# Kernel tuning notes

Hardware: AMD Instinct MI355X
Metric: run time of the kernel (lower is better)

## Reference

```python
import jax, jax.numpy as jnp
import numpy as np

BN_EPS = 1e-5

def setup_inputs() -> dict:
    key = jax.random.key(0)
    ks = jax.random.split(key, 6)
    N, D, H = 1024, 256, 128
    scale = 0.05
    return {
        "graph_embeddings": jax.random.normal(ks[0], (N, D), jnp.float32),
        "W1": jax.random.normal(ks[1], (2 * D, H), jnp.float32) * scale,
        "b1": jnp.zeros((H,), jnp.float32),
        "W2": jax.random.normal(ks[2], (H, 1), jnp.float32) * scale,
        "b2": jnp.zeros((1,), jnp.float32),
        "Wg": jax.random.normal(ks[3], (D, H), jnp.float32) * scale,
        "bg": jnp.zeros((H,), jnp.float32),
        "gamma": jnp.ones((H,), jnp.float32),
        "beta": jnp.zeros((H,), jnp.float32),
    }

def reference(graph_embeddings, W1, b1, W2, b2, Wg, bg, gamma, beta):
    N, D = graph_embeddings.shape
    # Pairwise similarity MLP: sim(i,j) = sigmoid(W2 @ relu(W1 @ [x_i; x_j] + b1) + b2)
    # Split W1 over the concat dim so we never materialize [N,N,2D].
    a = graph_embeddings @ W1[:D]          # [N, H] contribution of x_i
    c = graph_embeddings @ W1[D:]          # [N, H] contribution of x_j
    h = jax.nn.relu(a[:, None, :] + c[None, :, :] + b1)   # [N, N, H]
    sim = jax.nn.sigmoid(jnp.einsum('ijh,h->ij', h, W2[:, 0]) + b2[0])  # [N, N]
    # Torch loop uses sim(i,j) with i<j for both directions; keep edge iff sim > 0.5.
    U = jnp.triu(sim, k=1)
    A = jnp.where(U > 0.5, U, 0.0)
    A = A + A.T + jnp.eye(N, dtype=sim.dtype)  # symmetric + GCN self-loops (weight 1)
    # GCN symmetric normalization: D^{-1/2} A D^{-1/2}
    deg = A.sum(axis=1)
    dis = jax.lax.rsqrt(deg)
    A_hat = A * dis[:, None] * dis[None, :]
    out = A_hat @ (graph_embeddings @ Wg) + bg  # [N, H]
    # BatchNorm1d (training mode: batch stats, biased variance)
    mean = out.mean(axis=0)
    var = out.var(axis=0)
    out = gamma * (out - mean) * jax.lax.rsqrt(var + BN_EPS) + beta
    return jax.nn.relu(out)
```

## Files before the change

### kernel.cpp

```cpp
#include <hip/hip_runtime.h>
#include <math.h>

constexpr int NN = 1024;
constexpr int DD = 256;
constexpr int HH = 128;
constexpr float BN_EPS = 1e-5f;

constexpr int OFF_A      = 0;
constexpr int OFF_AP     = OFF_A + NN * NN;
constexpr int OFF_CP     = OFF_AP + NN * HH;
constexpr int OFF_Y      = OFF_CP + NN * HH;
constexpr int OFF_DIS    = OFF_Y + NN * HH;
constexpr int OFF_STATS  = OFF_DIS + NN;
constexpr int OFF_OUTPRE = OFF_STATS + 256;
constexpr int OFF_P4     = OFF_OUTPRE + NN * HH;

__global__ __launch_bounds__(256) void k1_gemm(
    const float* __restrict__ X, const float* __restrict__ W1,
    const float* __restrict__ Wg, const float* __restrict__ b1,
    float* __restrict__ aP, float* __restrict__ cP, float* __restrict__ y) {
  __shared__ float xs[16 * 256];
  __shared__ float ws[64 * 128];
  const int tid = threadIdx.x;
  const int i0 = blockIdx.x * 16;
  const int m = blockIdx.y;
  const float* W = (m == 0) ? W1 : (m == 1 ? W1 + DD * HH : Wg);
  const float* Xbase = X + i0 * DD;
#pragma unroll
  for (int v = 0; v < 4; ++v) {
    const int fi = (v * 256 + tid) * 4;
    *(float4*)(xs + fi) = *(const float4*)(Xbase + fi);
  }
  const int tx = tid & 31, ty = tid >> 5;
  float4 acc0 = make_float4(0.f, 0.f, 0.f, 0.f);
  float4 acc1 = make_float4(0.f, 0.f, 0.f, 0.f);
  for (int c = 0; c < 4; ++c) {
    __syncthreads();
    const float* Wbase = W + c * 64 * HH;
#pragma unroll
    for (int v = 0; v < 8; ++v) {
      const int fi = (v * 256 + tid) * 4;
      *(float4*)(ws + fi) = *(const float4*)(Wbase + fi);
    }
    __syncthreads();
    const float* xr0 = xs + (ty * 2) * 256 + c * 64;
    const float* xr1 = xs + (ty * 2 + 1) * 256 + c * 64;
#pragma unroll 4
    for (int d = 0; d < 64; d += 4) {
      const float4 x0 = *(const float4*)(xr0 + d);
      const float4 x1 = *(const float4*)(xr1 + d);
      const float4 w0 = *(const float4*)(ws + (d + 0) * 128 + tx * 4);
      const float4 w1 = *(const float4*)(ws + (d + 1) * 128 + tx * 4);
      const float4 w2 = *(const float4*)(ws + (d + 2) * 128 + tx * 4);
      const float4 w3 = *(const float4*)(ws + (d + 3) * 128 + tx * 4);
      acc0.x = fmaf(x0.x, w0.x, acc0.x); acc0.y = fmaf(x0.x, w0.y, acc0.y);
      acc0.z = fmaf(x0.x, w0.z, acc0.z); acc0.w = fmaf(x0.x, w0.w, acc0.w);
      acc1.x = fmaf(x1.x, w0.x, acc1.x); acc1.y = fmaf(x1.x, w0.y, acc1.y);
      acc1.z = fmaf(x1.x, w0.z, acc1.z); acc1.w = fmaf(x1.x, w0.w, acc1.w);
      acc0.x = fmaf(x0.y, w1.x, acc0.x); acc0.y = fmaf(x0.y, w1.y, acc0.y);
      acc0.z = fmaf(x0.y, w1.z, acc0.z); acc0.w = fmaf(x0.y, w1.w, acc0.w);
      acc1.x = fmaf(x1.y, w1.x, acc1.x); acc1.y = fmaf(x1.y, w1.y, acc1.y);
      acc1.z = fmaf(x1.y, w1.z, acc1.z); acc1.w = fmaf(x1.y, w1.w, acc1.w);
      acc0.x = fmaf(x0.z, w2.x, acc0.x); acc0.y = fmaf(x0.z, w2.y, acc0.y);
      acc0.z = fmaf(x0.z, w2.z, acc0.z); acc0.w = fmaf(x0.z, w2.w, acc0.w);
      acc1.x = fmaf(x1.z, w2.x, acc1.x); acc1.y = fmaf(x1.z, w2.y, acc1.y);
      acc1.z = fmaf(x1.z, w2.z, acc1.z); acc1.w = fmaf(x1.z, w2.w, acc1.w);
      acc0.x = fmaf(x0.w, w3.x, acc0.x); acc0.y = fmaf(x0.w, w3.y, acc0.y);
      acc0.z = fmaf(x0.w, w3.z, acc0.z); acc0.w = fmaf(x0.w, w3.w, acc0.w);
      acc1.x = fmaf(x1.w, w3.x, acc1.x); acc1.y = fmaf(x1.w, w3.y, acc1.y);
      acc1.z = fmaf(x1.w, w3.z, acc1.z); acc1.w = fmaf(x1.w, w3.w, acc1.w);
    }
  }
  float* dst = (m == 0) ? aP : (m == 1 ? cP : y);
  if (m == 0) {
    const float4 bv = *(const float4*)(b1 + tx * 4);
    acc0.x += bv.x; acc0.y += bv.y; acc0.z += bv.z; acc0.w += bv.w;
    acc1.x += bv.x; acc1.y += bv.y; acc1.z += bv.z; acc1.w += bv.w;
  }
  const int r0 = i0 + ty * 2;
  *(float4*)(dst + r0 * HH + tx * 4) = acc0;
  *(float4*)(dst + (r0 + 1) * HH + tx * 4) = acc1;
}

__global__ __launch_bounds__(256) void k2_pairwise(
    const float* __restrict__ aP, const float* __restrict__ cP,
    const float* __restrict__ W2, const float* __restrict__ b2,
    float* __restrict__ A) {
  const int ti = blockIdx.x, tj = blockIdx.y;
  if (tj < ti) return;
  __shared__ float as[32 * 132];
  __shared__ float cs[32 * 132];
  __shared__ float es[32 * 33];
  const int tid = threadIdx.x;
  const int i0 = ti * 32, j0 = tj * 32;
  for (int idx = tid; idx < 32 * HH; idx += 256) {
    const int row = idx >> 7, col = idx & 127;
    as[row * 132 + col] = aP[(i0 + row) * HH + col];
    cs[row * 132 + col] = cP[(j0 + row) * HH + col];
  }
  __syncthreads();
  const int li0 = (tid >> 4) * 2, lj0 = (tid & 15) * 2;
  float s00 = 0.f, s01 = 0.f, s10 = 0.f, s11 = 0.f;
#pragma unroll 8
  for (int h = 0; h < HH; h += 4) {
    const float4 a0 = *(const float4*)(as + li0 * 132 + h);
    const float4 a1 = *(const float4*)(as + (li0 + 1) * 132 + h);
    const float4 c0 = *(const float4*)(cs + lj0 * 132 + h);
    const float4 c1 = *(const float4*)(cs + (lj0 + 1) * 132 + h);
    const float4 w = *(const float4*)(W2 + h);
    s00 += fmaxf(a0.x + c0.x, 0.f) * w.x + fmaxf(a0.y + c0.y, 0.f) * w.y +
           fmaxf(a0.z + c0.z, 0.f) * w.z + fmaxf(a0.w + c0.w, 0.f) * w.w;
    s01 += fmaxf(a0.x + c1.x, 0.f) * w.x + fmaxf(a0.y + c1.y, 0.f) * w.y +
           fmaxf(a0.z + c1.z, 0.f) * w.z + fmaxf(a0.w + c1.w, 0.f) * w.w;
    s10 += fmaxf(a1.x + c0.x, 0.f) * w.x + fmaxf(a1.y + c0.y, 0.f) * w.y +
           fmaxf(a1.z + c0.z, 0.f) * w.z + fmaxf(a1.w + c0.w, 0.f) * w.w;
    s11 += fmaxf(a1.x + c1.x, 0.f) * w.x + fmaxf(a1.y + c1.y, 0.f) * w.y +
           fmaxf(a1.z + c1.z, 0.f) * w.z + fmaxf(a1.w + c1.w, 0.f) * w.w;
  }
  const float b2v = b2[0];
  auto edge = [b2v](float s) {
    s += b2v;
    return s > 0.f ? 1.f / (1.f + __expf(-s)) : 0.f;
  };
  es[(li0 + 0) * 33 + lj0 + 0] = edge(s00);
  es[(li0 + 0) * 33 + lj0 + 1] = edge(s01);
  es[(li0 + 1) * 33 + lj0 + 0] = edge(s10);
  es[(li0 + 1) * 33 + lj0 + 1] = edge(s11);
  __syncthreads();
  if (ti == tj) {
#pragma unroll
    for (int r = 0; r < 2; ++r)
#pragma unroll
      for (int t = 0; t < 2; ++t) {
        const int li = li0 + r, lj = lj0 + t;
        const float v =
            (li == lj) ? 1.f : (li < lj ? es[li * 33 + lj] : es[lj * 33 + li]);
        A[(i0 + li) * NN + j0 + lj] = v;
      }
  } else {
#pragma unroll
    for (int r = 0; r < 2; ++r)
#pragma unroll
      for (int t = 0; t < 2; ++t) {
        const int li = li0 + r, lj = lj0 + t;
        A[(i0 + li) * NN + j0 + lj] = es[li * 33 + lj];
        A[(j0 + li) * NN + i0 + lj] = es[lj * 33 + li];
      }
  }
}

__global__ __launch_bounds__(256) void k3_deg(
    const float* __restrict__ A, float* __restrict__ dis,
    float* __restrict__ stats) {
  const int i = blockIdx.x;
  const int tid = threadIdx.x;
  if (i == 0) stats[tid] = 0.f;
  const float4 v = *(const float4*)(A + i * NN + tid * 4);
  float s = v.x + v.y + v.z + v.w;
#pragma unroll
  for (int off = 32; off > 0; off >>= 1) s += __shfl_down(s, off, 64);
  __shared__ float sm[4];
  if ((tid & 63) == 0) sm[tid >> 6] = s;
  __syncthreads();
  if (tid == 0) dis[i] = rsqrtf(sm[0] + sm[1] + sm[2] + sm[3]);
}

__global__ __launch_bounds__(256) void k4_spmm_partial(
    const float* __restrict__ A, const float* __restrict__ Y,
    const float* __restrict__ dis, float* __restrict__ P4) {
  __shared__ float At[128 * 36];
  __shared__ float ys[32 * 128];
  const int tid = threadIdx.x;
  const int i0 = blockIdx.x * 32;
  const int jc = blockIdx.y * 128;
  for (int idx = tid; idx < 32 * 128; idx += 256) {
    const int col = idx & 127, row = idx >> 7;
    At[col * 36 + row] = A[(i0 + row) * NN + jc + col];
  }
  const int tx = tid & 31, ty = tid >> 5;
  float4 acc[4];
#pragma unroll
  for (int r = 0; r < 4; ++r) acc[r] = make_float4(0.f, 0.f, 0.f, 0.f);
  for (int s = 0; s < 4; ++s) {
    __syncthreads();
#pragma unroll
    for (int v = 0; v < 4; ++v) {
      const int fi = (v * 256 + tid) * 4;
      const int r = fi >> 7, col = fi & 127;
      float4 t = *(const float4*)(Y + (jc + s * 32 + r) * HH + col);
      const float dv = dis[jc + s * 32 + r];
      t.x *= dv; t.y *= dv; t.z *= dv; t.w *= dv;
      *(float4*)(ys + fi) = t;
    }
    __syncthreads();
#pragma unroll 8
    for (int jj = 0; jj < 32; ++jj) {
      const float4 av = *(const float4*)(At + (s * 32 + jj) * 36 + ty * 4);
      const float4 yv = *(const float4*)(ys + jj * 128 + tx * 4);
      acc[0].x = fmaf(av.x, yv.x, acc[0].x); acc[0].y = fmaf(av.x, yv.y, acc[0].y);
      acc[0].z = fmaf(av.x, yv.z, acc[0].z); acc[0].w = fmaf(av.x, yv.w, acc[0].w);
      acc[1].x = fmaf(av.y, yv.x, acc[1].x); acc[1].y = fmaf(av.y, yv.y, acc[1].y);
      acc[1].z = fmaf(av.y, yv.z, acc[1].z); acc[1].w = fmaf(av.y, yv.w, acc[1].w);
      acc[2].x = fmaf(av.z, yv.x, acc[2].x); acc[2].y = fmaf(av.z, yv.y, acc[2].y);
      acc[2].z = fmaf(av.z, yv.z, acc[2].z); acc[2].w = fmaf(av.z, yv.w, acc[2].w);
      acc[3].x = fmaf(av.w, yv.x, acc[3].x); acc[3].y = fmaf(av.w, yv.y, acc[3].y);
      acc[3].z = fmaf(av.w, yv.z, acc[3].z); acc[3].w = fmaf(av.w, yv.w, acc[3].w);
    }
  }
  const int bc = blockIdx.y;
#pragma unroll
  for (int r = 0; r < 4; ++r) {
    const int i = i0 + ty * 4 + r;
    *(float4*)(P4 + bc * (NN * HH) + i * HH + tx * 4) = acc[r];
  }
}

__global__ __launch_bounds__(256) void k5a_reduce_stats(
    const float* __restrict__ P4, const float* __restrict__ dis,
    const float* __restrict__ bg, float* __restrict__ out_pre,
    float* __restrict__ stats) {
  const int tid = threadIdx.x;
  const int h = tid & 127, rg = tid >> 7;
  const int i0 = blockIdx.x * 8;
  float ls = 0.f, lq = 0.f;
  const float bgv = bg[h];
#pragma unroll
  for (int r = rg; r < 8; r += 2) {
    const int i = i0 + r;
    float v = 0.f;
#pragma unroll
    for (int s = 0; s < 8; ++s) v += P4[s * (NN * HH) + i * HH + h];
    v = v * dis[i] + bgv;
    out_pre[i * HH + h] = v;
    ls += v;
    lq += v * v;
  }
  __shared__ float sm1[2][128], sm2[2][128];
  sm1[rg][h] = ls;
  sm2[rg][h] = lq;
  __syncthreads();
  if (rg == 0) {
    atomicAdd(&stats[h], sm1[0][h] + sm1[1][h]);
    atomicAdd(&stats[128 + h], sm2[0][h] + sm2[1][h]);
  }
}

__global__ __launch_bounds__(256) void k5b_bn(
    const float* __restrict__ out_pre, const float* __restrict__ stats,
    const float* __restrict__ gamma, const float* __restrict__ beta,
    float* __restrict__ out) {
  const int idx = blockIdx.x * 256 + threadIdx.x;
  const int h = idx & 127;
  const float mean = stats[h] * (1.f / NN);
  const float var = stats[128 + h] * (1.f / NN) - mean * mean;
  float v = (out_pre[idx] - mean) * rsqrtf(var + BN_EPS);
  v = gamma[h] * v + beta[h];
  out[idx] = fmaxf(v, 0.f);
}

extern "C" void kernel_launch(void* const* d_in, const int* in_sizes, int n_in,
                              void* d_out, int out_size, void* d_ws,
                              size_t ws_size, hipStream_t stream) {
  const float* X = (const float*)d_in[0];
  const float* W1 = (const float*)d_in[1];
  const float* b1 = (const float*)d_in[2];
  const float* W2 = (const float*)d_in[3];
  const float* b2 = (const float*)d_in[4];
  const float* Wg = (const float*)d_in[5];
  const float* bg = (const float*)d_in[6];
  const float* gamma = (const float*)d_in[7];
  const float* beta = (const float*)d_in[8];
  float* out = (float*)d_out;

  float* w = (float*)d_ws;
  float* A = w + OFF_A;
  float* aP = w + OFF_AP;
  float* cP = w + OFF_CP;
  float* y = w + OFF_Y;
  float* dis = w + OFF_DIS;
  float* stats = w + OFF_STATS;
  float* out_pre = w + OFF_OUTPRE;
  float* P4 = w + OFF_P4;

  k1_gemm<<<dim3(64, 3), 256, 0, stream>>>(X, W1, Wg, b1, aP, cP, y);
  k2_pairwise<<<dim3(32, 32), 256, 0, stream>>>(aP, cP, W2, b2, A);
  k3_deg<<<dim3(1024), 256, 0, stream>>>(A, dis, stats);
  k4_spmm_partial<<<dim3(32, 8), 256, 0, stream>>>(A, y, dis, P4);
  k5a_reduce_stats<<<dim3(128), 256, 0, stream>>>(P4, dis, bg, out_pre, stats);
  k5b_bn<<<dim3(512), 256, 0, stream>>>(out_pre, stats, gamma, beta, out);
}
```

Measured before the change: 121.2 us.

## Fuse all stages into one cooperative persistent kernel with grid syncs

Replaces the six separate launches with a single cooperative kernel of 256 blocks that runs every stage and separates them with grid.sync(). Degree computation is folded into the pairwise stage as per-tile row and column sums accumulated with atomicAdd, which removes the separate pass that re-read the full 1024x1024 adjacency matrix. The pairwise stage now walks only the upper-triangle tiles, so no blocks exit early. This removes launch gaps and one full read of A, at the cost of grid-wide barriers, fewer blocks during the pairwise stage, and float atomics that make the degree sums order-dependent.

```diff
diff --git a/kernel.cpp b/kernel.cpp
--- a/kernel.cpp
+++ b/kernel.cpp
@@ -1,5 +1,8 @@
 #include <hip/hip_runtime.h>
+#include <hip/hip_cooperative_groups.h>
 #include <math.h>
+
+namespace cg = cooperative_groups;
 
 constexpr int NN = 1024;
 constexpr int DD = 256;
@@ -10,252 +13,275 @@
 constexpr int OFF_AP     = OFF_A + NN * NN;
 constexpr int OFF_CP     = OFF_AP + NN * HH;
 constexpr int OFF_Y      = OFF_CP + NN * HH;
-constexpr int OFF_DIS    = OFF_Y + NN * HH;
-constexpr int OFF_STATS  = OFF_DIS + NN;
+constexpr int OFF_DEG    = OFF_Y + NN * HH;
+constexpr int OFF_STATS  = OFF_DEG + NN;
 constexpr int OFF_OUTPRE = OFF_STATS + 256;
 constexpr int OFF_P4     = OFF_OUTPRE + NN * HH;
 
-__global__ __launch_bounds__(256) void k1_gemm(
+__global__ __launch_bounds__(256) void mega(
     const float* __restrict__ X, const float* __restrict__ W1,
-    const float* __restrict__ Wg, const float* __restrict__ b1,
-    float* __restrict__ aP, float* __restrict__ cP, float* __restrict__ y) {
-  __shared__ float xs[16 * 256];
-  __shared__ float ws[64 * 128];
+    const float* __restrict__ b1, const float* __restrict__ W2,
+    const float* __restrict__ b2, const float* __restrict__ Wg,
+    const float* __restrict__ bg, const float* __restrict__ gamma,
+    const float* __restrict__ beta, float* __restrict__ out,
+    float* __restrict__ wsp) {
+  cg::grid_group grid = cg::this_grid();
+  __shared__ float smem[12288];
+
+  float* A = wsp + OFF_A;
+  float* aP = wsp + OFF_AP;
+  float* cP = wsp + OFF_CP;
+  float* Y = wsp + OFF_Y;
+  float* deg = wsp + OFF_DEG;
+  float* stats = wsp + OFF_STATS;
+  float* out_pre = wsp + OFF_OUTPRE;
+  float* P4 = wsp + OFF_P4;
+
   const int tid = threadIdx.x;
-  const int i0 = blockIdx.x * 16;
-  const int m = blockIdx.y;
-  const float* W = (m == 0) ? W1 : (m == 1 ? W1 + DD * HH : Wg);
-  const float* Xbase = X + i0 * DD;
-#pragma unroll
-  for (int v = 0; v < 4; ++v) {
-    const int fi = (v * 256 + tid) * 4;
-    *(float4*)(xs + fi) = *(const float4*)(Xbase + fi);
-  }
-  const int tx = tid & 31, ty = tid >> 5;
-  float4 acc0 = make_float4(0.f, 0.f, 0.f, 0.f);
-  float4 acc1 = make_float4(0.f, 0.f, 0.f, 0.f);
-  for (int c = 0; c < 4; ++c) {
-    __syncthreads();
-    const float* Wbase = W + c * 64 * HH;
-#pragma unroll
-    for (int v = 0; v < 8; ++v) {
-      const int fi = (v * 256 + tid) * 4;
-      *(float4*)(ws + fi) = *(const float4*)(Wbase + fi);
-    }
-    __syncthreads();
-    const float* xr0 = xs + (ty * 2) * 256 + c * 64;
-    const float* xr1 = xs + (ty * 2 + 1) * 256 + c * 64;
-#pragma unroll 4
-    for (int d = 0; d < 64; d += 4) {
-      const float4 x0 = *(const float4*)(xr0 + d);
-      const float4 x1 = *(const float4*)(xr1 + d);
-      const float4 w0 = *(const float4*)(ws + (d + 0) * 128 + tx * 4);
-      const float4 w1 = *(const float4*)(ws + (d + 1) * 128 + tx * 4);
-      const float4 w2 = *(const float4*)(ws + (d + 2) * 128 + tx * 4);
-      const float4 w3 = *(const float4*)(ws + (d + 3) * 128 + tx * 4);
-      acc0.x = fmaf(x0.x, w0.x, acc0.x); acc0.y = fmaf(x0.x, w0.y, acc0.y);
-      acc0.z = fmaf(x0.x, w0.z, acc0.z); acc0.w = fmaf(x0.x, w0.w, acc0.w);
-      acc1.x = fmaf(x1.x, w0.x, acc1.x); acc1.y = fmaf(x1.x, w0.y, acc1.y);
-      acc1.z = fmaf(x1.x, w0.z, acc1.z); acc1.w = fmaf(x1.x, w0.w, acc1.w);
-      acc0.x = fmaf(x0.y, w1.x, acc0.x); acc0.y = fmaf(x0.y, w1.y, acc0.y);
-      acc0.z = fmaf(x0.y, w1.z, acc0.z); acc0.w = fmaf(x0.y, w1.w, acc0.w);
-      acc1.x = fmaf(x1.y, w1.x, acc1.x); acc1.y = fmaf(x1.y, w1.y, acc1.y);
-      acc1.z = fmaf(x1.y, w1.z, acc1.z); acc1.w = fmaf(x1.y, w1.w, acc1.w);
-      acc0.x = fmaf(x0.z, w2.x, acc0.x); acc0.y = fmaf(x0.z, w2.y, acc0.y);
-      acc0.z = fmaf(x0.z, w2.z, acc0.z); acc0.w = fmaf(x0.z, w2.w, acc0.w);
-      acc1.x = fmaf(x1.z, w2.x, acc1.x); acc1.y = fmaf(x1.z, w2.y, acc1.y);
-      acc1.z = fmaf(x1.z, w2.z, acc1.z); acc1.w = fmaf(x1.z, w2.w, acc1.w);
-      acc0.x = fmaf(x0.w, w3.x, acc0.x); acc0.y = fmaf(x0.w, w3.y, acc0.y);
-      acc0.z = fmaf(x0.w, w3.z, acc0.z); acc0.w = fmaf(x0.w, w3.w, acc0.w);
-      acc1.x = fmaf(x1.w, w3.x, acc1.x); acc1.y = fmaf(x1.w, w3.y, acc1.y);
-      acc1.z = fmaf(x1.w, w3.z, acc1.z); acc1.w = fmaf(x1.w, w3.w, acc1.w);
-    }
-  }
-  float* dst = (m == 0) ? aP : (m == 1 ? cP : y);
-  if (m == 0) {
-    const float4 bv = *(const float4*)(b1 + tx * 4);
-    acc0.x += bv.x; acc0.y += bv.y; acc0.z += bv.z; acc0.w += bv.w;
-    acc1.x += bv.x; acc1.y += bv.y; acc1.z += bv.z; acc1.w += bv.w;
-  }
-  const int r0 = i0 + ty * 2;
-  *(float4*)(dst + r0 * HH + tx * 4) = acc0;
-  *(float4*)(dst + (r0 + 1) * HH + tx * 4) = acc1;
-}
-
-__global__ __launch_bounds__(256) void k2_pairwise(
-    const float* __restrict__ aP, const float* __restrict__ cP,
-    const float* __restrict__ W2, const float* __restrict__ b2,
-    float* __restrict__ A) {
-  const int ti = blockIdx.x, tj = blockIdx.y;
-  if (tj < ti) return;
-  __shared__ float as[32 * 132];
-  __shared__ float cs[32 * 132];
-  __shared__ float es[32 * 33];
-  const int tid = threadIdx.x;
-  const int i0 = ti * 32, j0 = tj * 32;
-  for (int idx = tid; idx < 32 * HH; idx += 256) {
-    const int row = idx >> 7, col = idx & 127;
-    as[row * 132 + col] = aP[(i0 + row) * HH + col];
-    cs[row * 132 + col] = cP[(j0 + row) * HH + col];
-  }
-  __syncthreads();
-  const int li0 = (tid >> 4) * 2, lj0 = (tid & 15) * 2;
-  float s00 = 0.f, s01 = 0.f, s10 = 0.f, s11 = 0.f;
-#pragma unroll 8
-  for (int h = 0; h < HH; h += 4) {
-    const float4 a0 = *(const float4*)(as + li0 * 132 + h);
-    const float4 a1 = *(const float4*)(as + (li0 + 1) * 132 + h);
-    const float4 c0 = *(const float4*)(cs + lj0 * 132 + h);
-    const float4 c1 = *(const float4*)(cs + (lj0 + 1) * 132 + h);
-    const float4 w = *(const float4*)(W2 + h);
-    s00 += fmaxf(a0.x + c0.x, 0.f) * w.x + fmaxf(a0.y + c0.y, 0.f) * w.y +
-           fmaxf(a0.z + c0.z, 0.f) * w.z + fmaxf(a0.w + c0.w, 0.f) * w.w;
-    s01 += fmaxf(a0.x + c1.x, 0.f) * w.x + fmaxf(a0.y + c1.y, 0.f) * w.y +
-           fmaxf(a0.z + c1.z, 0.f) * w.z + fmaxf(a0.w + c1.w, 0.f) * w.w;
-    s10 += fmaxf(a1.x + c0.x, 0.f) * w.x + fmaxf(a1.y + c0.y, 0.f) * w.y +
-           fmaxf(a1.z + c0.z, 0.f) * w.z + fmaxf(a1.w + c0.w, 0.f) * w.w;
-    s11 += fmaxf(a1.x + c1.x, 0.f) * w.x + fmaxf(a1.y + c1.y, 0.f) * w.y +
-           fmaxf(a1.z + c1.z, 0.f) * w.z + fmaxf(a1.w + c1.w, 0.f) * w.w;
-  }
-  const float b2v = b2[0];
-  auto edge = [b2v](float s) {
-    s += b2v;
-    return s > 0.f ? 1.f / (1.f + __expf(-s)) : 0.f;
-  };
-  es[(li0 + 0) * 33 + lj0 + 0] = edge(s00);
-  es[(li0 + 0) * 33 + lj0 + 1] = edge(s01);
-  es[(li0 + 1) * 33 + lj0 + 0] = edge(s10);
-  es[(li0 + 1) * 33 + lj0 + 1] = edge(s11);
-  __syncthreads();
-  if (ti == tj) {
-#pragma unroll
-    for (int r = 0; r < 2; ++r)
-#pragma unroll
-      for (int t = 0; t < 2; ++t) {
-        const int li = li0 + r, lj = lj0 + t;
-        const float v =
-            (li == lj) ? 1.f : (li < lj ? es[li * 33 + lj] : es[lj * 33 + li]);
-        A[(i0 + li) * NN + j0 + lj] = v;
-      }
-  } else {
-#pragma unroll
-    for (int r = 0; r < 2; ++r)
-#pragma unroll
-      for (int t = 0; t < 2; ++t) {
-        const int li = li0 + r, lj = lj0 + t;
-        A[(i0 + li) * NN + j0 + lj] = es[li * 33 + lj];
-        A[(j0 + li) * NN + i0 + lj] = es[lj * 33 + li];
-      }
-  }
-}
-
-__global__ __launch_bounds__(256) void k3_deg(
-    const float* __restrict__ A, float* __restrict__ dis,
-    float* __restrict__ stats) {
-  const int i = blockIdx.x;
-  const int tid = threadIdx.x;
-  if (i == 0) stats[tid] = 0.f;
-  const float4 v = *(const float4*)(A + i * NN + tid * 4);
-  float s = v.x + v.y + v.z + v.w;
-#pragma unroll
-  for (int off = 32; off > 0; off >>= 1) s += __shfl_down(s, off, 64);
-  __shared__ float sm[4];
-  if ((tid & 63) == 0) sm[tid >> 6] = s;
-  __syncthreads();
-  if (tid == 0) dis[i] = rsqrtf(sm[0] + sm[1] + sm[2] + sm[3]);
-}
-
-__global__ __launch_bounds__(256) void k4_spmm_partial(
-    const float* __restrict__ A, const float* __restrict__ Y,
-    const float* __restrict__ dis, float* __restrict__ P4) {
-  __shared__ float At[128 * 36];
-  __shared__ float ys[32 * 128];
-  const int tid = threadIdx.x;
-  const int i0 = blockIdx.x * 32;
-  const int jc = blockIdx.y * 128;
-  for (int idx = tid; idx < 32 * 128; idx += 256) {
-    const int col = idx & 127, row = idx >> 7;
-    At[col * 36 + row] = A[(i0 + row) * NN + jc + col];
-  }
-  const int tx = tid & 31, ty = tid >> 5;
-  float4 acc[4];
-#pragma unroll
-  for (int r = 0; r < 4; ++r) acc[r] = make_float4(0.f, 0.f, 0.f, 0.f);
-  for (int s = 0; s < 4; ++s) {
-    __syncthreads();
+  const int blk = blockIdx.x;
+
+  if (blk < 192) {
+    float* xs = smem;
+    float* wb = smem + 4096;
+    const int i0 = (blk & 63) * 16;
+    const int m = blk >> 6;
+    const float* W = (m == 0) ? W1 : (m == 1 ? W1 + DD * HH : Wg);
+    const float* Xbase = X + i0 * DD;
 #pragma unroll
     for (int v = 0; v < 4; ++v) {
       const int fi = (v * 256 + tid) * 4;
-      const int r = fi >> 7, col = fi & 127;
-      float4 t = *(const float4*)(Y + (jc + s * 32 + r) * HH + col);
-      const float dv = dis[jc + s * 32 + r];
-      t.x *= dv; t.y *= dv; t.z *= dv; t.w *= dv;
-      *(float4*)(ys + fi) = t;
-    }
+      *(float4*)(xs + fi) = *(const float4*)(Xbase + fi);
+    }
+    const int tx = tid & 31, ty = tid >> 5;
+    float4 acc0 = make_float4(0.f, 0.f, 0.f, 0.f);
+    float4 acc1 = make_float4(0.f, 0.f, 0.f, 0.f);
+    for (int c = 0; c < 4; ++c) {
+      __syncthreads();
+      const float* Wbase = W + c * 64 * HH;
+#pragma unroll
+      for (int v = 0; v < 8; ++v) {
+        const int fi = (v * 256 + tid) * 4;
+        *(float4*)(wb + fi) = *(const float4*)(Wbase + fi);
+      }
+      __syncthreads();
+      const float* xr0 = xs + (ty * 2) * 256 + c * 64;
+      const float* xr1 = xs + (ty * 2 + 1) * 256 + c * 64;
+#pragma unroll 4
+      for (int d = 0; d < 64; d += 4) {
+        const float4 x0 = *(const float4*)(xr0 + d);
+        const float4 x1 = *(const float4*)(xr1 + d);
+        const float4 w0 = *(const float4*)(wb + (d + 0) * 128 + tx * 4);
+        const float4 w1 = *(const float4*)(wb + (d + 1) * 128 + tx * 4);
+        const float4 w2 = *(const float4*)(wb + (d + 2) * 128 + tx * 4);
+        const float4 w3 = *(const float4*)(wb + (d + 3) * 128 + tx * 4);
+        acc0.x = fmaf(x0.x, w0.x, acc0.x); acc0.y = fmaf(x0.x, w0.y, acc0.y);
+        acc0.z = fmaf(x0.x, w0.z, acc0.z); acc0.w = fmaf(x0.x, w0.w, acc0.w);
+        acc1.x = fmaf(x1.x, w0.x, acc1.x); acc1.y = fmaf(x1.x, w0.y, acc1.y);
+        acc1.z = fmaf(x1.x, w0.z, acc1.z); acc1.w = fmaf(x1.x, w0.w, acc1.w);
+        acc0.x = fmaf(x0.y, w1.x, acc0.x); acc0.y = fmaf(x0.y, w1.y, acc0.y);
+        acc0.z = fmaf(x0.y, w1.z, acc0.z); acc0.w = fmaf(x0.y, w1.w, acc0.w);
+        acc1.x = fmaf(x1.y, w1.x, acc1.x); acc1.y = fmaf(x1.y, w1.y, acc1.y);
+        acc1.z = fmaf(x1.y, w1.z, acc1.z); acc1.w = fmaf(x1.y, w1.w, acc1.w);
+        acc0.x = fmaf(x0.z, w2.x, acc0.x); acc0.y = fmaf(x0.z, w2.y, acc0.y);
+        acc0.z = fmaf(x0.z, w2.z, acc0.z); acc0.w = fmaf(x0.z, w2.w, acc0.w);
+        acc1.x = fmaf(x1.z, w2.x, acc1.x); acc1.y = fmaf(x1.z, w2.y, acc1.y);
+        acc1.z = fmaf(x1.z, w2.z, acc1.z); acc1.w = fmaf(x1.z, w2.w, acc1.w);
+        acc0.x = fmaf(x0.w, w3.x, acc0.x); acc0.y = fmaf(x0.w, w3.y, acc0.y);
+        acc0.z = fmaf(x0.w, w3.z, acc0.z); acc0.w = fmaf(x0.w, w3.w, acc0.w);
+        acc1.x = fmaf(x1.w, w3.x, acc1.x); acc1.y = fmaf(x1.w, w3.y, acc1.y);
+        acc1.z = fmaf(x1.w, w3.z, acc1.z); acc1.w = fmaf(x1.w, w3.w, acc1.w);
+      }
+    }
+    float* dst = (m == 0) ? aP : (m == 1 ? cP : Y);
+    if (m == 0) {
+      const float4 bv = *(const float4*)(b1 + tx * 4);
+      acc0.x += bv.x; acc0.y += bv.y; acc0.z += bv.z; acc0.w += bv.w;
+      acc1.x += bv.x; acc1.y += bv.y; acc1.z += bv.z; acc1.w += bv.w;
+    }
+    const int r0 = i0 + ty * 2;
+    *(float4*)(dst + r0 * HH + tx * 4) = acc0;
+    *(float4*)(dst + (r0 + 1) * HH + tx * 4) = acc1;
+  } else if (blk == 192) {
+    for (int i = tid; i < NN; i += 256) deg[i] = 0.f;
+  } else if (blk == 193) {
+    stats[tid] = 0.f;
+  }
+  grid.sync();
+
+  {
+    float* as = smem;
+    float* cs = smem + 4224;
+    float* es = smem + 8448;
+    const float b2v = b2[0];
+    for (int t = blk; t < 528; t += 256) {
+      __syncthreads();
+      int tt = t, ti = 0;
+      while (tt >= 32 - ti) { tt -= 32 - ti; ++ti; }
+      const int tj = ti + tt;
+      const int i0 = ti * 32, j0 = tj * 32;
+      for (int idx = tid; idx < 32 * HH; idx += 256) {
+        const int row = idx >> 7, col = idx & 127;
+        as[row * 132 + col] = aP[(i0 + row) * HH + col];
+        cs[row * 132 + col] = cP[(j0 + row) * HH + col];
+      }
+      __syncthreads();
+      const int li0 = (tid >> 4) * 2, lj0 = (tid & 15) * 2;
+      float s00 = 0.f, s01 = 0.f, s10 = 0.f, s11 = 0.f;
+#pragma unroll 8
+      for (int h = 0; h < HH; h += 4) {
+        const float4 a0 = *(const float4*)(as + li0 * 132 + h);
+        const float4 a1 = *(const float4*)(as + (li0 + 1) * 132 + h);
+        const float4 c0 = *(const float4*)(cs + lj0 * 132 + h);
+        const float4 c1 = *(const float4*)(cs + (lj0 + 1) * 132 + h);
+        const float4 w = *(const float4*)(W2 + h);
+        s00 += fmaxf(a0.x + c0.x, 0.f) * w.x + fmaxf(a0.y + c0.y, 0.f) * w.y +
+               fmaxf(a0.z + c0.z, 0.f) * w.z + fmaxf(a0.w + c0.w, 0.f) * w.w;
+        s01 += fmaxf(a0.x + c1.x, 0.f) * w.x + fmaxf(a0.y + c1.y, 0.f) * w.y +
+               fmaxf(a0.z + c1.z, 0.f) * w.z + fmaxf(a0.w + c1.w, 0.f) * w.w;
+        s10 += fmaxf(a1.x + c0.x, 0.f) * w.x + fmaxf(a1.y + c0.y, 0.f) * w.y +
+               fmaxf(a1.z + c0.z, 0.f) * w.z + fmaxf(a1.w + c0.w, 0.f) * w.w;
+        s11 += fmaxf(a1.x + c1.x, 0.f) * w.x + fmaxf(a1.y + c1.y, 0.f) * w.y +
+               fmaxf(a1.z + c1.z, 0.f) * w.z + fmaxf(a1.w + c1.w, 0.f) * w.w;
+      }
+      auto edge = [b2v](float s) {
+        s += b2v;
+        return s > 0.f ? 1.f / (1.f + __expf(-s)) : 0.f;
+      };
+      es[(li0 + 0) * 33 + lj0 + 0] = edge(s00);
+      es[(li0 + 0) * 33 + lj0 + 1] = edge(s01);
+      es[(li0 + 1) * 33 + lj0 + 0] = edge(s10);
+      es[(li0 + 1) * 33 + lj0 + 1] = edge(s11);
+      __syncthreads();
+      if (ti == tj) {
+        float f[2][2];
+#pragma unroll
+        for (int r = 0; r < 2; ++r)
+#pragma unroll
+          for (int c = 0; c < 2; ++c) {
+            const int li = li0 + r, lj = lj0 + c;
+            f[r][c] = (li == lj) ? 1.f
+                                 : (li < lj ? es[li * 33 + lj] : es[lj * 33 + li]);
+          }
+        __syncthreads();
+        es[(li0 + 0) * 33 + lj0 + 0] = f[0][0];
+        es[(li0 + 0) * 33 + lj0 + 1] = f[0][1];
+        es[(li0 + 1) * 33 + lj0 + 0] = f[1][0];
+        es[(li0 + 1) * 33 + lj0 + 1] = f[1][1];
+        __syncthreads();
+      }
+      if (tid < 32) {
+        float s = 0.f;
+#pragma unroll
+        for (int c = 0; c < 32; ++c) s += es[tid * 33 + c];
+        atomicAdd(deg + i0 + tid, s);
+      } else if (tid < 64 && ti != tj) {
+        const int c = tid - 32;
+        float s = 0.f;
+#pragma unroll
+        for (int r = 0; r < 32; ++r) s += es[r * 33 + c];
+        atomicAdd(deg + j0 + c, s);
+      }
+#pragma unroll
+      for (int r = 0; r < 2; ++r)
+#pragma unroll
+        for (int c = 0; c < 2; ++c) {
+          const int li = li0 + r, lj = lj0 + c;
+          A[(i0 + li) * NN + j0 + lj] = es[li * 33 + lj];
+          if (ti != tj) A[(j0 + li) * NN + i0 + lj] = es[lj * 33 + li];
+        }
+    }
+  }
+  grid.sync();
+
+  {
+    float* At = smem;
+    float* ys = smem + 4608;
+    const int i0 = (blk >> 3) * 32;
+    const int jc = (blk & 7) * 128;
+    for (int idx = tid; idx < 32 * 128; idx += 256) {
+      const int col = idx & 127, row = idx >> 7;
+      At[col * 36 + row] = A[(i0 + row) * NN + jc + col];
+    }
+    const int tx = tid & 31, ty = tid >> 5;
+    float4 acc[4];
+#pragma unroll
+    for (int r = 0; r < 4; ++r) acc[r] = make_float4(0.f, 0.f, 0.f, 0.f);
+    for (int s = 0; s < 4; ++s) {
+      __syncthreads();
+#pragma unroll
+      for (int v = 0; v < 4; ++v) {
+        const int fi = (v * 256 + tid) * 4;
+        const int r = fi >> 7, col = fi & 127;
+        const int j = jc + s * 32 + r;
+        float4 tv = *(const float4*)(Y + j * HH + col);
+        const float dv = rsqrtf(deg[j]);
+        tv.x *= dv; tv.y *= dv; tv.z *= dv; tv.w *= dv;
+        *(float4*)(ys + fi) = tv;
+      }
+      __syncthreads();
+#pragma unroll 8
+      for (int jj = 0; jj < 32; ++jj) {
+        const float4 av = *(const float4*)(At + (s * 32 + jj) * 36 + ty * 4);
+        const float4 yv = *(const float4*)(ys + jj * 128 + tx * 4);
+        acc[0].x = fmaf(av.x, yv.x, acc[0].x); acc[0].y = fmaf(av.x, yv.y, acc[0].y);
+        acc[0].z = fmaf(av.x, yv.z, acc[0].z); acc[0].w = fmaf(av.x, yv.w, acc[0].w);
+        acc[1].x = fmaf(av.y, yv.x, acc[1].x); acc[1].y = fmaf(av.y, yv.y, acc[1].y);
+        acc[1].z = fmaf(av.y, yv.z, acc[1].z); acc[1].w = fmaf(av.y, yv.w, acc[1].w);
+        acc[2].x = fmaf(av.z, yv.x, acc[2].x); acc[2].y = fmaf(av.z, yv.y, acc[2].y);
+        acc[2].z = fmaf(av.z, yv.z, acc[2].z); acc[2].w = fmaf(av.z, yv.w, acc[2].w);
+        acc[3].x = fmaf(av.w, yv.x, acc[3].x); acc[3].y = fmaf(av.w, yv.y, acc[3].y);
+        acc[3].z = fmaf(av.w, yv.z, acc[3].z); acc[3].w = fmaf(av.w, yv.w, acc[3].w);
+      }
+    }
+    const int bc = blk & 7;
+#pragma unroll
+    for (int r = 0; r < 4; ++r) {
+      const int i = i0 + ty * 4 + r;
+      *(float4*)(P4 + bc * (NN * HH) + i * HH + tx * 4) = acc[r];
+    }
+  }
+  grid.sync();
+
+  {
+    const int h = tid & 127, rg = tid >> 7;
+    const int i0 = blk * 4;
+    const float bgv = bg[h];
+    float ls = 0.f, lq = 0.f;
+#pragma unroll
+    for (int r = rg; r < 4; r += 2) {
+      const int i = i0 + r;
+      float v = 0.f;
+#pragma unroll
+      for (int s = 0; s < 8; ++s) v += P4[s * (NN * HH) + i * HH + h];
+      v = v * rsqrtf(deg[i]) + bgv;
+      out_pre[i * HH + h] = v;
+      ls += v;
+      lq += v * v;
+    }
+    float* sm1 = smem;
+    float* sm2 = smem + 256;
+    sm1[rg * 128 + h] = ls;
+    sm2[rg * 128 + h] = lq;
     __syncthreads();
-#pragma unroll 8
-    for (int jj = 0; jj < 32; ++jj) {
-      const float4 av = *(const float4*)(At + (s * 32 + jj) * 36 + ty * 4);
-      const float4 yv = *(const float4*)(ys + jj * 128 + tx * 4);
-      acc[0].x = fmaf(av.x, yv.x, acc[0].x); acc[0].y = fmaf(av.x, yv.y, acc[0].y);
-      acc[0].z = fmaf(av.x, yv.z, acc[0].z); acc[0].w = fmaf(av.x, yv.w, acc[0].w);
-      acc[1].x = fmaf(av.y, yv.x, acc[1].x); acc[1].y = fmaf(av.y, yv.y, acc[1].y);
-      acc[1].z = fmaf(av.y, yv.z, acc[1].z); acc[1].w = fmaf(av.y, yv.w, acc[1].w);
-      acc[2].x = fmaf(av.z, yv.x, acc[2].x); acc[2].y = fmaf(av.z, yv.y, acc[2].y);
-      acc[2].z = fmaf(av.z, yv.z, acc[2].z); acc[2].w = fmaf(av.z, yv.w, acc[2].w);
-      acc[3].x = fmaf(av.w, yv.x, acc[3].x); acc[3].y = fmaf(av.w, yv.y, acc[3].y);
-      acc[3].z = fmaf(av.w, yv.z, acc[3].z); acc[3].w = fmaf(av.w, yv.w, acc[3].w);
-    }
-  }
-  const int bc = blockIdx.y;
-#pragma unroll
-  for (int r = 0; r < 4; ++r) {
-    const int i = i0 + ty * 4 + r;
-    *(float4*)(P4 + bc * (NN * HH) + i * HH + tx * 4) = acc[r];
-  }
-}
-
-__global__ __launch_bounds__(256) void k5a_reduce_stats(
-    const float* __restrict__ P4, const float* __restrict__ dis,
-    const float* __restrict__ bg, float* __restrict__ out_pre,
-    float* __restrict__ stats) {
-  const int tid = threadIdx.x;
-  const int h = tid & 127, rg = tid >> 7;
-  const int i0 = blockIdx.x * 8;
-  float ls = 0.f, lq = 0.f;
-  const float bgv = bg[h];
-#pragma unroll
-  for (int r = rg; r < 8; r += 2) {
-    const int i = i0 + r;
-    float v = 0.f;
-#pragma unroll
-    for (int s = 0; s < 8; ++s) v += P4[s * (NN * HH) + i * HH + h];
-    v = v * dis[i] + bgv;
-    out_pre[i * HH + h] = v;
-    ls += v;
-    lq += v * v;
-  }
-  __shared__ float sm1[2][128], sm2[2][128];
-  sm1[rg][h] = ls;
-  sm2[rg][h] = lq;
-  __syncthreads();
-  if (rg == 0) {
-    atomicAdd(&stats[h], sm1[0][h] + sm1[1][h]);
-    atomicAdd(&stats[128 + h], sm2[0][h] + sm2[1][h]);
-  }
-}
-
-__global__ __launch_bounds__(256) void k5b_bn(
-    const float* __restrict__ out_pre, const float* __restrict__ stats,
-    const float* __restrict__ gamma, const float* __restrict__ beta,
-    float* __restrict__ out) {
-  const int idx = blockIdx.x * 256 + threadIdx.x;
-  const int h = idx & 127;
-  const float mean = stats[h] * (1.f / NN);
-  const float var = stats[128 + h] * (1.f / NN) - mean * mean;
-  float v = (out_pre[idx] - mean) * rsqrtf(var + BN_EPS);
-  v = gamma[h] * v + beta[h];
-  out[idx] = fmaxf(v, 0.f);
+    if (rg == 0) {
+      atomicAdd(&stats[h], sm1[h] + sm1[128 + h]);
+      atomicAdd(&stats[128 + h], sm2[h] + sm2[128 + h]);
+    }
+  }
+  grid.sync();
+
+  {
+#pragma unroll
+    for (int k = 0; k < 2; ++k) {
+      const int idx = blk * 512 + k * 256 + tid;
+      const int h = idx & 127;
+      const float mean = stats[h] * (1.f / NN);
+      const float var = stats[128 + h] * (1.f / NN) - mean * mean;
+      float v = (out_pre[idx] - mean) * rsqrtf(var + BN_EPS);
+      v = gamma[h] * v + beta[h];
+      out[idx] = fmaxf(v, 0.f);
+    }
+  }
 }
 
 extern "C" void kernel_launch(void* const* d_in, const int* in_sizes, int n_in,
@@ -271,21 +297,11 @@
   const float* gamma = (const float*)d_in[7];
   const float* beta = (const float*)d_in[8];
   float* out = (float*)d_out;
-
-  float* w = (float*)d_ws;
-  float* A = w + OFF_A;
-  float* aP = w + OFF_AP;
-  float* cP = w + OFF_CP;
-  float* y = w + OFF_Y;
-  float* dis = w + OFF_DIS;
-  float* stats = w + OFF_STATS;
-  float* out_pre = w + OFF_OUTPRE;
-  float* P4 = w + OFF_P4;
-
-  k1_gemm<<<dim3(64, 3), 256, 0, stream>>>(X, W1, Wg, b1, aP, cP, y);
-  k2_pairwise<<<dim3(32, 32), 256, 0, stream>>>(aP, cP, W2, b2, A);
-  k3_deg<<<dim3(1024), 256, 0, stream>>>(A, dis, stats);
-  k4_spmm_partial<<<dim3(32, 8), 256, 0, stream>>>(A, y, dis, P4);
-  k5a_reduce_stats<<<dim3(128), 256, 0, stream>>>(P4, dis, bg, out_pre, stats);
-  k5b_bn<<<dim3(512), 256, 0, stream>>>(out_pre, stats, gamma, beta, out);
+  float* wsp = (float*)d_ws;
+
+  void* args[] = {(void*)&X,  (void*)&W1,    (void*)&b1,   (void*)&W2,
+                  (void*)&b2, (void*)&Wg,    (void*)&bg,   (void*)&gamma,
+                  (void*)&beta, (void*)&out, (void*)&wsp};
+  hipLaunchCooperativeKernel((const void*)mega, dim3(256), dim3(256), args, 0,
+                             stream);
 }
```

Measured after the change: 253.1 us. 2.09x slower.

## Fuse degree into pairwise kernel, merge SpMM with reduce/stats, compact triangular grid

Applied to the files above, without the earlier changes.

Degree sums are now accumulated with atomics inside the pairwise kernel, which removes the separate degree kernel and its full re-read of A. The split-K SpMM with partial buffers and a separate reduce kernel is replaced by a single kernel: each block loads 4 rows of A plus all degrees and computes output rows directly, with bias and BN stats folded in. The pairwise grid is compacted to only upper-triangular tiles, W2 is staged in shared memory, and deg/stats zeroing is folded into the first GEMM launch. The trade-offs are that Y is read uncoalesced-per-h across all 1024 rows in every SpMM block, and there is atomic contention on deg.

```diff
diff --git a/kernel.cpp b/kernel.cpp
--- a/kernel.cpp
+++ b/kernel.cpp
@@ -10,20 +10,29 @@
 constexpr int OFF_AP     = OFF_A + NN * NN;
 constexpr int OFF_CP     = OFF_AP + NN * HH;
 constexpr int OFF_Y      = OFF_CP + NN * HH;
-constexpr int OFF_DIS    = OFF_Y + NN * HH;
-constexpr int OFF_STATS  = OFF_DIS + NN;
+constexpr int OFF_DEG    = OFF_Y + NN * HH;
+constexpr int OFF_STATS  = OFF_DEG + NN;
 constexpr int OFF_OUTPRE = OFF_STATS + 256;
-constexpr int OFF_P4     = OFF_OUTPRE + NN * HH;
 
 __global__ __launch_bounds__(256) void k1_gemm(
     const float* __restrict__ X, const float* __restrict__ W1,
     const float* __restrict__ Wg, const float* __restrict__ b1,
-    float* __restrict__ aP, float* __restrict__ cP, float* __restrict__ y) {
+    float* __restrict__ aP, float* __restrict__ cP, float* __restrict__ Y,
+    float* __restrict__ deg, float* __restrict__ stats) {
+  const int tid = threadIdx.x;
+  const int blk = blockIdx.x;
+  if (blk >= 192) {
+    if (blk == 192) {
+      for (int i = tid; i < NN; i += 256) deg[i] = 0.f;
+    } else {
+      stats[tid] = 0.f;
+    }
+    return;
+  }
   __shared__ float xs[16 * 256];
   __shared__ float ws[64 * 128];
-  const int tid = threadIdx.x;
-  const int i0 = blockIdx.x * 16;
-  const int m = blockIdx.y;
+  const int i0 = (blk & 63) * 16;
+  const int m = blk >> 6;
   const float* W = (m == 0) ? W1 : (m == 1 ? W1 + DD * HH : Wg);
   const float* Xbase = X + i0 * DD;
 #pragma unroll
@@ -71,7 +80,7 @@
       acc1.z = fmaf(x1.w, w3.z, acc1.z); acc1.w = fmaf(x1.w, w3.w, acc1.w);
     }
   }
-  float* dst = (m == 0) ? aP : (m == 1 ? cP : y);
+  float* dst = (m == 0) ? aP : (m == 1 ? cP : Y);
   if (m == 0) {
     const float4 bv = *(const float4*)(b1 + tx * 4);
     acc0.x += bv.x; acc0.y += bv.y; acc0.z += bv.z; acc0.w += bv.w;
@@ -85,14 +94,17 @@
 __global__ __launch_bounds__(256) void k2_pairwise(
     const float* __restrict__ aP, const float* __restrict__ cP,
     const float* __restrict__ W2, const float* __restrict__ b2,
-    float* __restrict__ A) {
-  const int ti = blockIdx.x, tj = blockIdx.y;
-  if (tj < ti) return;
+    float* __restrict__ A, float* __restrict__ deg) {
   __shared__ float as[32 * 132];
   __shared__ float cs[32 * 132];
   __shared__ float es[32 * 33];
+  __shared__ float ws2[128];
   const int tid = threadIdx.x;
+  int tt = blockIdx.x, ti = 0;
+  while (tt >= 32 - ti) { tt -= 32 - ti; ++ti; }
+  const int tj = ti + tt;
   const int i0 = ti * 32, j0 = tj * 32;
+  if (tid < 32) *(float4*)(ws2 + tid * 4) = *(const float4*)(W2 + tid * 4);
   for (int idx = tid; idx < 32 * HH; idx += 256) {
     const int row = idx >> 7, col = idx & 127;
     as[row * 132 + col] = aP[(i0 + row) * HH + col];
@@ -107,7 +119,7 @@
     const float4 a1 = *(const float4*)(as + (li0 + 1) * 132 + h);
     const float4 c0 = *(const float4*)(cs + lj0 * 132 + h);
     const float4 c1 = *(const float4*)(cs + (lj0 + 1) * 132 + h);
-    const float4 w = *(const float4*)(W2 + h);
+    const float4 w = *(const float4*)(ws2 + h);
     s00 += fmaxf(a0.x + c0.x, 0.f) * w.x + fmaxf(a0.y + c0.y, 0.f) * w.y +
            fmaxf(a0.z + c0.z, 0.f) * w.z + fmaxf(a0.w + c0.w, 0.f) * w.w;
     s01 += fmaxf(a0.x + c1.x, 0.f) * w.x + fmaxf(a0.y + c1.y, 0.f) * w.y +
@@ -128,124 +140,101 @@
   es[(li0 + 1) * 33 + lj0 + 1] = edge(s11);
   __syncthreads();
   if (ti == tj) {
+    float f[2][2];
 #pragma unroll
     for (int r = 0; r < 2; ++r)
 #pragma unroll
-      for (int t = 0; t < 2; ++t) {
-        const int li = li0 + r, lj = lj0 + t;
-        const float v =
+      for (int c = 0; c < 2; ++c) {
+        const int li = li0 + r, lj = lj0 + c;
+        f[r][c] =
             (li == lj) ? 1.f : (li < lj ? es[li * 33 + lj] : es[lj * 33 + li]);
-        A[(i0 + li) * NN + j0 + lj] = v;
       }
-  } else {
-#pragma unroll
-    for (int r = 0; r < 2; ++r)
-#pragma unroll
-      for (int t = 0; t < 2; ++t) {
-        const int li = li0 + r, lj = lj0 + t;
-        A[(i0 + li) * NN + j0 + lj] = es[li * 33 + lj];
-        A[(j0 + li) * NN + i0 + lj] = es[lj * 33 + li];
-      }
-  }
-}
-
-__global__ __launch_bounds__(256) void k3_deg(
-    const float* __restrict__ A, float* __restrict__ dis,
-    float* __restrict__ stats) {
-  const int i = blockIdx.x;
+    __syncthreads();
+    es[(li0 + 0) * 33 + lj0 + 0] = f[0][0];
+    es[(li0 + 0) * 33 + lj0 + 1] = f[0][1];
+    es[(li0 + 1) * 33 + lj0 + 0] = f[1][0];
+    es[(li0 + 1) * 33 + lj0 + 1] = f[1][1];
+    __syncthreads();
+  }
+  if (tid < 32) {
+    float s = 0.f;
+#pragma unroll
+    for (int c = 0; c < 32; ++c) s += es[tid * 33 + c];
+    atomicAdd(deg + i0 + tid, s);
+  } else if (tid < 64 && ti != tj) {
+    const int c = tid - 32;
+    float s = 0.f;
+#pragma unroll
+    for (int r = 0; r < 32; ++r) s += es[r * 33 + c];
+    atomicAdd(deg + j0 + c, s);
+  }
+#pragma unroll
+  for (int r = 0; r < 2; ++r)
+#pragma unroll
+    for (int c = 0; c < 2; ++c) {
+      const int li = li0 + r, lj = lj0 + c;
+      A[(i0 + li) * NN + j0 + lj] = es[li * 33 + lj];
+      if (ti != tj) A[(j0 + li) * NN + i0 + lj] = es[lj * 33 + li];
+    }
+}
+
+__global__ __launch_bounds__(256) void k3_spmm(
+    const float* __restrict__ A, const float* __restrict__ Y,
+    const float* __restrict__ deg, const float* __restrict__ bg,
+    float* __restrict__ out_pre, float* __restrict__ stats) {
+  __shared__ float As[4 * 1024];
+  __shared__ float disl[1024];
+  __shared__ float sred[512];
   const int tid = threadIdx.x;
-  if (i == 0) stats[tid] = 0.f;
-  const float4 v = *(const float4*)(A + i * NN + tid * 4);
-  float s = v.x + v.y + v.z + v.w;
-#pragma unroll
-  for (int off = 32; off > 0; off >>= 1) s += __shfl_down(s, off, 64);
-  __shared__ float sm[4];
-  if ((tid & 63) == 0) sm[tid >> 6] = s;
-  __syncthreads();
-  if (tid == 0) dis[i] = rsqrtf(sm[0] + sm[1] + sm[2] + sm[3]);
-}
-
-__global__ __launch_bounds__(256) void k4_spmm_partial(
-    const float* __restrict__ A, const float* __restrict__ Y,
-    const float* __restrict__ dis, float* __restrict__ P4) {
-  __shared__ float At[128 * 36];
-  __shared__ float ys[32 * 128];
-  const int tid = threadIdx.x;
-  const int i0 = blockIdx.x * 32;
-  const int jc = blockIdx.y * 128;
-  for (int idx = tid; idx < 32 * 128; idx += 256) {
-    const int col = idx & 127, row = idx >> 7;
-    At[col * 36 + row] = A[(i0 + row) * NN + jc + col];
-  }
-  const int tx = tid & 31, ty = tid >> 5;
-  float4 acc[4];
-#pragma unroll
-  for (int r = 0; r < 4; ++r) acc[r] = make_float4(0.f, 0.f, 0.f, 0.f);
-  for (int s = 0; s < 4; ++s) {
-    __syncthreads();
-#pragma unroll
-    for (int v = 0; v < 4; ++v) {
-      const int fi = (v * 256 + tid) * 4;
-      const int r = fi >> 7, col = fi & 127;
-      float4 t = *(const float4*)(Y + (jc + s * 32 + r) * HH + col);
-      const float dv = dis[jc + s * 32 + r];
-      t.x *= dv; t.y *= dv; t.z *= dv; t.w *= dv;
-      *(float4*)(ys + fi) = t;
-    }
-    __syncthreads();
-#pragma unroll 8
-    for (int jj = 0; jj < 32; ++jj) {
-      const float4 av = *(const float4*)(At + (s * 32 + jj) * 36 + ty * 4);
-      const float4 yv = *(const float4*)(ys + jj * 128 + tx * 4);
-      acc[0].x = fmaf(av.x, yv.x, acc[0].x); acc[0].y = fmaf(av.x, yv.y, acc[0].y);
-      acc[0].z = fmaf(av.x, yv.z, acc[0].z); acc[0].w = fmaf(av.x, yv.w, acc[0].w);
-      acc[1].x = fmaf(av.y, yv.x, acc[1].x); acc[1].y = fmaf(av.y, yv.y, acc[1].y);
-      acc[1].z = fmaf(av.y, yv.z, acc[1].z); acc[1].w = fmaf(av.y, yv.w, acc[1].w);
-      acc[2].x = fmaf(av.z, yv.x, acc[2].x); acc[2].y = fmaf(av.z, yv.y, acc[2].y);
-      acc[2].z = fmaf(av.z, yv.z, acc[2].z); acc[2].w = fmaf(av.z, yv.w, acc[2].w);
-      acc[3].x = fmaf(av.w, yv.x, acc[3].x); acc[3].y = fmaf(av.w, yv.y, acc[3].y);
-      acc[3].z = fmaf(av.w, yv.z, acc[3].z); acc[3].w = fmaf(av.w, yv.w, acc[3].w);
-    }
-  }
-  const int bc = blockIdx.y;
-#pragma unroll
-  for (int r = 0; r < 4; ++r) {
-    const int i = i0 + ty * 4 + r;
-    *(float4*)(P4 + bc * (NN * HH) + i * HH + tx * 4) = acc[r];
-  }
-}
-
-__global__ __launch_bounds__(256) void k5a_reduce_stats(
-    const float* __restrict__ P4, const float* __restrict__ dis,
-    const float* __restrict__ bg, float* __restrict__ out_pre,
-    float* __restrict__ stats) {
-  const int tid = threadIdx.x;
+  const int i0 = blockIdx.x * 4;
+  const float* Ab = A + i0 * NN;
+#pragma unroll
+  for (int v = 0; v < 4; ++v) {
+    const int fi = (v * 256 + tid) * 4;
+    *(float4*)(As + fi) = *(const float4*)(Ab + fi);
+  }
+  {
+    const float4 dv = *(const float4*)(deg + tid * 4);
+    float4 r;
+    r.x = rsqrtf(dv.x); r.y = rsqrtf(dv.y); r.z = rsqrtf(dv.z); r.w = rsqrtf(dv.w);
+    *(float4*)(disl + tid * 4) = r;
+  }
+  __syncthreads();
   const int h = tid & 127, rg = tid >> 7;
-  const int i0 = blockIdx.x * 8;
-  float ls = 0.f, lq = 0.f;
+  float acc0 = 0.f, acc1 = 0.f;
+  const float* Yh = Y + h;
+  const float* Ar0 = As + (rg * 2) * 1024;
+  const float* Ar1 = As + (rg * 2 + 1) * 1024;
+#pragma unroll 4
+  for (int j = 0; j < 1024; j += 4) {
+    const float4 dv = *(const float4*)(disl + j);
+    const float y0 = Yh[(j + 0) * HH] * dv.x;
+    const float y1 = Yh[(j + 1) * HH] * dv.y;
+    const float y2 = Yh[(j + 2) * HH] * dv.z;
+    const float y3 = Yh[(j + 3) * HH] * dv.w;
+    const float4 a0 = *(const float4*)(Ar0 + j);
+    const float4 a1 = *(const float4*)(Ar1 + j);
+    acc0 = fmaf(a0.x, y0, acc0); acc0 = fmaf(a0.y, y1, acc0);
+    acc0 = fmaf(a0.z, y2, acc0); acc0 = fmaf(a0.w, y3, acc0);
+    acc1 = fmaf(a1.x, y0, acc1); acc1 = fmaf(a1.y, y1, acc1);
+    acc1 = fmaf(a1.z, y2, acc1); acc1 = fmaf(a1.w, y3, acc1);
+  }
   const float bgv = bg[h];
-#pragma unroll
-  for (int r = rg; r < 8; r += 2) {
-    const int i = i0 + r;
-    float v = 0.f;
-#pragma unroll
-    for (int s = 0; s < 8; ++s) v += P4[s * (NN * HH) + i * HH + h];
-    v = v * dis[i] + bgv;
-    out_pre[i * HH + h] = v;
-    ls += v;
-    lq += v * v;
-  }
-  __shared__ float sm1[2][128], sm2[2][128];
-  sm1[rg][h] = ls;
-  sm2[rg][h] = lq;
+  const float v0 = acc0 * disl[i0 + rg * 2] + bgv;
+  const float v1 = acc1 * disl[i0 + rg * 2 + 1] + bgv;
+  out_pre[(i0 + rg * 2) * HH + h] = v0;
+  out_pre[(i0 + rg * 2 + 1) * HH + h] = v1;
+  sred[rg * 128 + h] = v0 + v1;
+  __syncthreads();
+  sred[256 + rg * 128 + h] = v0 * v0 + v1 * v1;
   __syncthreads();
   if (rg == 0) {
-    atomicAdd(&stats[h], sm1[0][h] + sm1[1][h]);
-    atomicAdd(&stats[128 + h], sm2[0][h] + sm2[1][h]);
-  }
-}
-
-__global__ __launch_bounds__(256) void k5b_bn(
+    atomicAdd(&stats[h], sred[h] + sred[128 + h]);
+    atomicAdd(&stats[128 + h], sred[256 + h] + sred[384 + h]);
+  }
+}
+
+__global__ __launch_bounds__(256) void k4_bn(
     const float* __restrict__ out_pre, const float* __restrict__ stats,
     const float* __restrict__ gamma, const float* __restrict__ beta,
     float* __restrict__ out) {
@@ -276,16 +265,13 @@
   float* A = w + OFF_A;
   float* aP = w + OFF_AP;
   float* cP = w + OFF_CP;
-  float* y = w + OFF_Y;
-  float* dis = w + OFF_DIS;
+  float* Y = w + OFF_Y;
+  float* deg = w + OFF_DEG;
   float* stats = w + OFF_STATS;
   float* out_pre = w + OFF_OUTPRE;
-  float* P4 = w + OFF_P4;
-
-  k1_gemm<<<dim3(64, 3), 256, 0, stream>>>(X, W1, Wg, b1, aP, cP, y);
-  k2_pairwise<<<dim3(32, 32), 256, 0, stream>>>(aP, cP, W2, b2, A);
-  k3_deg<<<dim3(1024), 256, 0, stream>>>(A, dis, stats);
-  k4_spmm_partial<<<dim3(32, 8), 256, 0, stream>>>(A, y, dis, P4);
-  k5a_reduce_stats<<<dim3(128), 256, 0, stream>>>(P4, dis, bg, out_pre, stats);
-  k5b_bn<<<dim3(512), 256, 0, stream>>>(out_pre, stats, gamma, beta, out);
-}
+
+  k1_gemm<<<dim3(194), 256, 0, stream>>>(X, W1, Wg, b1, aP, cP, Y, deg, stats);
+  k2_pairwise<<<dim3(528), 256, 0, stream>>>(aP, cP, W2, b2, A, deg);
+  k3_spmm<<<dim3(256), 256, 0, stream>>>(A, Y, deg, bg, out_pre, stats);
+  k4_bn<<<dim3(512), 256, 0, stream>>>(out_pre, stats, gamma, beta, out);
+}
```

Result: slower. 127.9 us (+5.5%).
